# Kernel optimization log

Measured on AMD Instinct MI355X. Metric: run time of the kernel, lower is better.

## Reference

```python
import jax, jax.numpy as jnp
import numpy as np

GS_ITERS = 10
GS_TAU = 0.5
NEG = -1e9
B, L, D, H = 4, 512, 64, 128


def gphi_scores(x, W1, b1, W2, b2):
    # Faithful to: concat([x_i, x_j]) -> Linear(2D,H) -> ReLU -> Linear(H,1).squeeze(-1)
    # Linear on the concat of [x_i, x_j] == x_i @ W1[:D] + x_j @ W1[D:] (fused, no [B,L,L,2D] tensor).
    d = x.shape[-1]
    pi = jnp.einsum('bld,dh->blh', x, W1[:d])   # row-index half of concat
    pj = jnp.einsum('bld,dh->blh', x, W1[d:])   # col-index half of concat
    h = jax.nn.relu(pi[:, :, None, :] + pj[:, None, :, :] + b1)  # [B,L,L,H]
    return jnp.einsum('blmh,h->blm', h, W2[:, 0]) + b2[0]        # [B,L,L]


def gumbel_sinkhorn(log_alpha, gumbel, pad_mask, tau, n_iters):
    # (scores + gumbel noise)/tau, mask padded rows/cols, alternate row/col log-normalization.
    la = (log_alpha + gumbel) / tau
    la = jnp.where(pad_mask, NEG, la)

    def step(la, _):
        la = la - jax.nn.logsumexp(la, axis=2, keepdims=True)  # row normalize
        la = la - jax.nn.logsumexp(la, axis=1, keepdims=True)  # col normalize
        la = jnp.where(pad_mask, NEG, la)
        return la, None

    la, _ = jax.lax.scan(step, la, None, length=n_iters)
    return jnp.exp(la)


def make_pad_mask(seq_lens, max_len):
    # mask_map logic: for a sequence of length s, rows < s have cols < s valid; rows >= s fully invalid.
    ar = jnp.arange(max_len)
    s = seq_lens[:, None, None]
    valid = (ar[None, :, None] < s) & (ar[None, None, :] < s)
    return ~valid  # True where gumbel-masked


def setup_inputs() -> dict:
    key = jax.random.key(0)
    ks = jax.random.split(key, 8)
    event_time = jax.random.uniform(ks[0], (B, L), dtype=jnp.float32) * 10.0
    event_type = jax.random.randint(ks[1], (B, L), 0, 50, dtype=jnp.int32)
    clean_enc_out = jax.random.normal(ks[2], (B, L, D), dtype=jnp.float32)
    seq_lens = jax.random.randint(ks[3], (B,), 1, L + 1, dtype=jnp.int32)
    u = jax.random.uniform(ks[4], (B, L, L), dtype=jnp.float32, minval=1e-6, maxval=1.0 - 1e-6)
    gumbel_noise = -jnp.log(-jnp.log(u))
    # gphi_mlp params (xavier-ish scaling)
    W1 = jax.random.normal(ks[5], (2 * D, H), dtype=jnp.float32) * (1.0 / np.sqrt(2 * D))
    b1 = jnp.full((H,), 0.01, dtype=jnp.float32)
    W2 = jax.random.normal(ks[6], (H, 1), dtype=jnp.float32) * (1.0 / np.sqrt(H))
    b2 = jnp.full((1,), 0.01, dtype=jnp.float32)
    return {"event_time": event_time, "event_type": event_type,
            "clean_enc_out": clean_enc_out, "seq_lens": seq_lens,
            "gumbel_noise": gumbel_noise, "W1": W1, "b1": b1, "W2": W2, "b2": b2}


def reference(event_time, event_type, clean_enc_out, seq_lens, gumbel_noise, W1, b1, W2, b2):
    pad_mask = make_pad_mask(seq_lens, event_time.shape[1])
    scores = gphi_scores(clean_enc_out, W1, b1, W2, b2)           # [B,L,L]
    perm = gumbel_sinkhorn(scores, gumbel_noise, pad_mask, GS_TAU, GS_ITERS)
    # same_perm_matrix=True, no_time_noise=True path
    types_permed = jnp.einsum('bl,blm->bm', event_type.astype(jnp.float32), perm)
    times_permed = jnp.einsum('bl,blm->bm', event_time, perm)
    return types_permed, times_permed, perm
```

## Files before the change

### kernel.cpp

```cpp
#include <hip/hip_runtime.h>
#include <hip/hip_bf16.h>
#include <cstdint>

#define BB 4
#define LL 512
#define DD 64
#define HH 128
#define NEGV -1000000000.0f

__device__ __forceinline__ void fma4(float4& a, float s, const float4& w) {
    a.x += s * w.x; a.y += s * w.y; a.z += s * w.z; a.w += s * w.w;
}
__device__ __forceinline__ float4 f4max(const float4 a, const float4 b) {
    return make_float4(fmaxf(a.x,b.x), fmaxf(a.y,b.y), fmaxf(a.z,b.z), fmaxf(a.w,b.w));
}
__device__ __forceinline__ float4 f4add(const float4 a, const float4 b) {
    return make_float4(a.x+b.x, a.y+b.y, a.z+b.z, a.w+b.w);
}
__device__ __forceinline__ float4 f4expsub(const float4 v, const float4 m) {
    return make_float4(__expf(v.x-m.x), __expf(v.y-m.y), __expf(v.z-m.z), __expf(v.w-m.w));
}
__device__ __forceinline__ float4 f4mul(const float4 a, const float4 b) {
    return make_float4(a.x*b.x, a.y*b.y, a.z*b.z, a.w*b.w);
}
__device__ __forceinline__ float4 f4log(const float4 a) {
    return make_float4(__logf(a.x), __logf(a.y), __logf(a.z), __logf(a.w));
}

__global__ __launch_bounds__(256) void k_pipj(
    const float* __restrict__ x, const float* __restrict__ W1,
    const float* __restrict__ b1, float* __restrict__ pi, float* __restrict__ pj)
{
    int t = threadIdx.x;
    int hq = t & 63;
    int rr = t >> 6;
    int half = hq >> 5;
    int hc = (hq & 31) << 2;
    int row0 = blockIdx.x * 8 + rr;

    const float* Wb = W1 + half * 64 * HH + hc;
    float4 acc0;
    if (half == 0) acc0 = *(const float4*)(b1 + hc);
    else           acc0 = make_float4(0.f, 0.f, 0.f, 0.f);
    float4 acc1 = acc0;

    const float* x0 = x + (size_t)row0 * DD;
    const float* x1 = x + (size_t)(row0 + 4) * DD;
    #pragma unroll 4
    for (int dq = 0; dq < 16; ++dq) {
        float4 xa = *(const float4*)(x0 + (dq << 2));
        float4 xb = *(const float4*)(x1 + (dq << 2));
        float4 w0 = *(const float4*)(Wb + (dq*4 + 0) * HH);
        float4 w1 = *(const float4*)(Wb + (dq*4 + 1) * HH);
        float4 w2 = *(const float4*)(Wb + (dq*4 + 2) * HH);
        float4 w3 = *(const float4*)(Wb + (dq*4 + 3) * HH);
        fma4(acc0, xa.x, w0); fma4(acc0, xa.y, w1); fma4(acc0, xa.z, w2); fma4(acc0, xa.w, w3);
        fma4(acc1, xb.x, w0); fma4(acc1, xb.y, w1); fma4(acc1, xb.z, w2); fma4(acc1, xb.w, w3);
    }
    float* dst = half ? pj : pi;
    *(float4*)(dst + (size_t)row0 * HH + hc)       = acc0;
    *(float4*)(dst + (size_t)(row0 + 4) * HH + hc) = acc1;
}

__global__ __launch_bounds__(256) void k_scores(
    const float* __restrict__ pig, const float* __restrict__ pjg,
    const float* __restrict__ W2g, const float* __restrict__ b2g,
    const float* __restrict__ gum, const int* __restrict__ slens,
    float* __restrict__ la)
{
    __shared__ float sp[64 * HH];
    __shared__ float sq[64 * HH];
    __shared__ float sw2[HH];

    int t = threadIdx.x;
    int b = blockIdx.z;
    int i0 = blockIdx.y * 64;
    int j0 = blockIdx.x * 64;
    int rowb = b * LL + i0;
    int colb = b * LL + j0;

    #pragma unroll
    for (int k = 0; k < 8; ++k) {
        int flat = (k << 8) + t;
        int i = flat >> 5;
        int q = flat & 31;
        int dq = q ^ ((i >> 2) & 7);
        float4 va = *(const float4*)(pig + ((size_t)(rowb + i)) * HH + (q << 2));
        float4 vb = *(const float4*)(pjg + ((size_t)(colb + i)) * HH + (q << 2));
        *(float4*)(sp + i * HH + (dq << 2)) = va;
        *(float4*)(sq + i * HH + (dq << 2)) = vb;
    }
    if (t < HH) sw2[t] = W2g[t];
    __syncthreads();

    int w = t >> 6, lane = t & 63;
    int ti = ((w >> 1) << 3) + (lane >> 3);
    int tj = ((w & 1) << 3) + (lane & 7);
    int kti = ti & 7, ktj = tj & 7;

    float acc[4][4];
    #pragma unroll
    for (int a = 0; a < 4; ++a)
        #pragma unroll
        for (int c = 0; c < 4; ++c) acc[a][c] = 0.f;

    for (int hq = 0; hq < 32; ++hq) {
        float4 w4 = *(const float4*)(sw2 + (hq << 2));
        int offi = (hq ^ kti) << 2;
        int offj = (hq ^ ktj) << 2;
        float4 pa[4], pb[4];
        #pragma unroll
        for (int a = 0; a < 4; ++a) pa[a] = *(const float4*)(sp + (4*ti + a) * HH + offi);
        #pragma unroll
        for (int c = 0; c < 4; ++c) pb[c] = *(const float4*)(sq + (4*tj + c) * HH + offj);
        #pragma unroll
        for (int a = 0; a < 4; ++a) {
            #pragma unroll
            for (int c = 0; c < 4; ++c) {
                float t0 = fmaxf(pa[a].x + pb[c].x, 0.f);
                float t1 = fmaxf(pa[a].y + pb[c].y, 0.f);
                float t2 = fmaxf(pa[a].z + pb[c].z, 0.f);
                float t3 = fmaxf(pa[a].w + pb[c].w, 0.f);
                float s = acc[a][c];
                s += t0 * w4.x; s += t1 * w4.y; s += t2 * w4.z; s += t3 * w4.w;
                acc[a][c] = s;
            }
        }
    }

    int sl = slens[b];
    float bb2 = b2g[0];
    int jb = j0 + 4 * tj;
    #pragma unroll
    for (int a = 0; a < 4; ++a) {
        int ig = i0 + 4 * ti + a;
        float4 g = *(const float4*)(gum + ((size_t)(b * LL + ig)) * LL + jb);
        bool iv = ig < sl;
        float4 o;
        o.x = (iv && (jb + 0) < sl) ? (acc[a][0] + bb2 + g.x) * 2.0f : NEGV;
        o.y = (iv && (jb + 1) < sl) ? (acc[a][1] + bb2 + g.y) * 2.0f : NEGV;
        o.z = (iv && (jb + 2) < sl) ? (acc[a][2] + bb2 + g.z) * 2.0f : NEGV;
        o.w = (iv && (jb + 3) < sl) ? (acc[a][3] + bb2 + g.w) * 2.0f : NEGV;
        *(float4*)(la + ((size_t)(b * LL + ig)) * LL + jb) = o;
    }
}

__global__ __launch_bounds__(256) void k_rownorm(float* __restrict__ la)
{
    int wid = (blockIdx.x << 2) + (threadIdx.x >> 6);
    int lane = threadIdx.x & 63;
    float4* row = (float4*)(la + (size_t)wid * LL);
    float4 a = row[lane];
    float4 b = row[lane + 64];
    float m = fmaxf(fmaxf(fmaxf(a.x, a.y), fmaxf(a.z, a.w)),
                    fmaxf(fmaxf(b.x, b.y), fmaxf(b.z, b.w)));
    #pragma unroll
    for (int off = 32; off; off >>= 1) m = fmaxf(m, __shfl_xor(m, off));
    float s = __expf(a.x - m) + __expf(a.y - m) + __expf(a.z - m) + __expf(a.w - m)
            + __expf(b.x - m) + __expf(b.y - m) + __expf(b.z - m) + __expf(b.w - m);
    #pragma unroll
    for (int off = 32; off; off >>= 1) s += __shfl_xor(s, off);
    float lse = m + __logf(s);
    a.x -= lse; a.y -= lse; a.z -= lse; a.w -= lse;
    b.x -= lse; b.y -= lse; b.z -= lse; b.w -= lse;
    row[lane] = a;
    row[lane + 64] = b;
}

__global__ __launch_bounds__(1024) void k_colnorm(
    float* __restrict__ la, const int* __restrict__ slens,
    const int* __restrict__ etype, const float* __restrict__ etime,
    float* __restrict__ otype, float* __restrict__ otime, int last)
{
    __shared__ float4 Lm[1024];
    __shared__ float4 Ls[1024];
    __shared__ float4 clse[8];

    int t = threadIdx.x;
    int cg = t & 7;
    int rg = t >> 3;
    int b  = blockIdx.x >> 4;
    int j0 = (blockIdx.x & 15) << 5;

    float4* base = (float4*)(la + ((size_t)b * LL) * LL + j0);

    float4 v[4];
    #pragma unroll
    for (int k = 0; k < 4; ++k) v[k] = base[(size_t)(4 * rg + k) * 128 + cg];

    float4 m = f4max(f4max(v[0], v[1]), f4max(v[2], v[3]));
    float4 s = f4add(f4add(f4expsub(v[0], m), f4expsub(v[1], m)),
                     f4add(f4expsub(v[2], m), f4expsub(v[3], m)));
    Lm[t] = m; Ls[t] = s;
    __syncthreads();
    for (int off = 64; off >= 1; off >>= 1) {
        if (rg < off) {
            float4 m2 = Lm[((rg + off) << 3) + cg];
            float4 s2 = Ls[((rg + off) << 3) + cg];
            float4 nm = f4max(m, m2);
            s = f4add(f4mul(s, f4expsub(m, nm)), f4mul(s2, f4expsub(m2, nm)));
            m = nm;
            Lm[t] = m; Ls[t] = s;
        }
        __syncthreads();
    }
    if (rg == 0) clse[cg] = f4add(m, f4log(s));
    __syncthreads();
    float4 lse = clse[cg];

    int sl = slens[b];
    int jb = j0 + (cg << 2);
    bool jv0 = (jb + 0) < sl, jv1 = (jb + 1) < sl, jv2 = (jb + 2) < sl, jv3 = (jb + 3) < sl;

    if (!last) {
        #pragma unroll
        for (int k = 0; k < 4; ++k) {
            int i = 4 * rg + k;
            bool iv = i < sl;
            float4 o;
            o.x = (iv && jv0) ? v[k].x - lse.x : NEGV;
            o.y = (iv && jv1) ? v[k].y - lse.y : NEGV;
            o.z = (iv && jv2) ? v[k].z - lse.z : NEGV;
            o.w = (iv && jv3) ? v[k].w - lse.w : NEGV;
            base[(size_t)i * 128 + cg] = o;
        }
    } else {
        float4 ty = make_float4(0.f, 0.f, 0.f, 0.f);
        float4 tm = make_float4(0.f, 0.f, 0.f, 0.f);
        #pragma unroll
        for (int k = 0; k < 4; ++k) {
            int i = 4 * rg + k;
            bool iv = i < sl;
            float etf = (float)etype[b * LL + i];
            float etm = etime[b * LL + i];
            float4 p;
            p.x = (iv && jv0) ? __expf(v[k].x - lse.x) : 0.f;
            p.y = (iv && jv1) ? __expf(v[k].y - lse.y) : 0.f;
            p.z = (iv && jv2) ? __expf(v[k].z - lse.z) : 0.f;
            p.w = (iv && jv3) ? __expf(v[k].w - lse.w) : 0.f;
            base[(size_t)i * 128 + cg] = p;
            fma4(ty, etf, p);
            fma4(tm, etm, p);
        }
        Lm[t] = ty; Ls[t] = tm;
        __syncthreads();
        for (int off = 64; off >= 1; off >>= 1) {
            if (rg < off) {
                ty = f4add(ty, Lm[((rg + off) << 3) + cg]);
                tm = f4add(tm, Ls[((rg + off) << 3) + cg]);
                Lm[t] = ty; Ls[t] = tm;
            }
            __syncthreads();
        }
        if (rg == 0) {
            *(float4*)(otype + b * LL + jb) = ty;
            *(float4*)(otime + b * LL + jb) = tm;
        }
    }
}

extern "C" void kernel_launch(void* const* d_in, const int* in_sizes, int n_in,
                              void* d_out, int out_size, void* d_ws, size_t ws_size,
                              hipStream_t stream)
{
    const float* etime = (const float*)d_in[0];
    const int*   etype = (const int*)d_in[1];
    const float* x     = (const float*)d_in[2];
    const int*   slens = (const int*)d_in[3];
    const float* gum   = (const float*)d_in[4];
    const float* W1    = (const float*)d_in[5];
    const float* b1    = (const float*)d_in[6];
    const float* W2    = (const float*)d_in[7];
    const float* b2    = (const float*)d_in[8];

    float* out   = (float*)d_out;
    float* otype = out;
    float* otime = out + BB * LL;
    float* la    = out + 2 * BB * LL;
    float* pi = (float*)d_ws;
    float* pj = pi + (size_t)BB * LL * HH;

    k_pipj<<<256, 256, 0, stream>>>(x, W1, b1, pi, pj);
    k_scores<<<dim3(8, 8, BB), 256, 0, stream>>>(pi, pj, W2, b2, gum, slens, la);
    for (int it = 0; it < 10; ++it) {
        k_rownorm<<<512, 256, 0, stream>>>(la);
        k_colnorm<<<64, 1024, 0, stream>>>(la, slens, etype, etime, otype, otime,
                                           (it == 9) ? 1 : 0);
    }
}
```

Before: 133.9 us.

## Fuse whole pipeline into one cooperative persistent kernel with grid barriers

Replaces the 22 separate launches (projection, scores, and ten row/column normalisation pairs) with a single cooperative kernel using atomic grid barriers between phases. During Sinkhorn, 64 blocks each keep a 32-row stripe of the score matrix resident in shared memory. Row normalisation is done locally, and column log-sum-exp is combined through partial max/sum buffers in global memory with one grid barrier per iteration. This removes launch overhead and repeated global round trips of the 4MB matrix, at the cost of idle blocks during Sinkhorn, spin-barrier latency, and reliance on co-residency of 256 blocks of 1024 threads.

```diff
diff --git a/kernel.cpp b/kernel.cpp
--- a/kernel.cpp
+++ b/kernel.cpp
@@ -1,5 +1,4 @@
 #include <hip/hip_runtime.h>
-#include <hip/hip_bf16.h>
 #include <cstdint>
 
 #define BB 4
@@ -7,255 +6,318 @@
 #define DD 64
 #define HH 128
 #define NEGV -1000000000.0f
-
-__device__ __forceinline__ void fma4(float4& a, float s, const float4& w) {
-    a.x += s * w.x; a.y += s * w.y; a.z += s * w.z; a.w += s * w.w;
+#define NBLK 256
+#define NTHR 1024
+#define NACT 64
+
+__device__ __forceinline__ void grid_barrier(unsigned* cnt, unsigned target) {
+    __syncthreads();
+    if (threadIdx.x == 0) {
+        __hip_atomic_fetch_add(cnt, 1u, __ATOMIC_RELEASE, __HIP_MEMORY_SCOPE_AGENT);
+        while (__hip_atomic_load(cnt, __ATOMIC_ACQUIRE, __HIP_MEMORY_SCOPE_AGENT) < target)
+            __builtin_amdgcn_s_sleep(2);
+    }
+    __syncthreads();
 }
-__device__ __forceinline__ float4 f4max(const float4 a, const float4 b) {
-    return make_float4(fmaxf(a.x,b.x), fmaxf(a.y,b.y), fmaxf(a.z,b.z), fmaxf(a.w,b.w));
+
+__device__ __forceinline__ float hmax4(float4 v) {
+    return fmaxf(fmaxf(v.x, v.y), fmaxf(v.z, v.w));
 }
-__device__ __forceinline__ float4 f4add(const float4 a, const float4 b) {
-    return make_float4(a.x+b.x, a.y+b.y, a.z+b.z, a.w+b.w);
-}
-__device__ __forceinline__ float4 f4expsub(const float4 v, const float4 m) {
-    return make_float4(__expf(v.x-m.x), __expf(v.y-m.y), __expf(v.z-m.z), __expf(v.w-m.w));
-}
-__device__ __forceinline__ float4 f4mul(const float4 a, const float4 b) {
-    return make_float4(a.x*b.x, a.y*b.y, a.z*b.z, a.w*b.w);
-}
-__device__ __forceinline__ float4 f4log(const float4 a) {
-    return make_float4(__logf(a.x), __logf(a.y), __logf(a.z), __logf(a.w));
-}
-
-__global__ __launch_bounds__(256) void k_pipj(
-    const float* __restrict__ x, const float* __restrict__ W1,
-    const float* __restrict__ b1, float* __restrict__ pi, float* __restrict__ pj)
+
+__global__ __launch_bounds__(NTHR) void mega(
+    const float* __restrict__ etime, const int* __restrict__ etype,
+    const float* __restrict__ x, const int* __restrict__ slens,
+    const float* __restrict__ gum, const float* __restrict__ W1,
+    const float* __restrict__ b1, const float* __restrict__ W2,
+    const float* __restrict__ b2, float* __restrict__ out, float* __restrict__ ws)
 {
-    int t = threadIdx.x;
-    int hq = t & 63;
-    int rr = t >> 6;
-    int half = hq >> 5;
-    int hc = (hq & 31) << 2;
-    int row0 = blockIdx.x * 8 + rr;
-
-    const float* Wb = W1 + half * 64 * HH + hc;
-    float4 acc0;
-    if (half == 0) acc0 = *(const float4*)(b1 + hc);
-    else           acc0 = make_float4(0.f, 0.f, 0.f, 0.f);
-    float4 acc1 = acc0;
-
-    const float* x0 = x + (size_t)row0 * DD;
-    const float* x1 = x + (size_t)(row0 + 4) * DD;
-    #pragma unroll 4
-    for (int dq = 0; dq < 16; ++dq) {
-        float4 xa = *(const float4*)(x0 + (dq << 2));
-        float4 xb = *(const float4*)(x1 + (dq << 2));
-        float4 w0 = *(const float4*)(Wb + (dq*4 + 0) * HH);
-        float4 w1 = *(const float4*)(Wb + (dq*4 + 1) * HH);
-        float4 w2 = *(const float4*)(Wb + (dq*4 + 2) * HH);
-        float4 w3 = *(const float4*)(Wb + (dq*4 + 3) * HH);
-        fma4(acc0, xa.x, w0); fma4(acc0, xa.y, w1); fma4(acc0, xa.z, w2); fma4(acc0, xa.w, w3);
-        fma4(acc1, xb.x, w0); fma4(acc1, xb.y, w1); fma4(acc1, xb.z, w2); fma4(acc1, xb.w, w3);
-    }
-    float* dst = half ? pj : pi;
-    *(float4*)(dst + (size_t)row0 * HH + hc)       = acc0;
-    *(float4*)(dst + (size_t)(row0 + 4) * HH + hc) = acc1;
-}
-
-__global__ __launch_bounds__(256) void k_scores(
-    const float* __restrict__ pig, const float* __restrict__ pjg,
-    const float* __restrict__ W2g, const float* __restrict__ b2g,
-    const float* __restrict__ gum, const int* __restrict__ slens,
-    float* __restrict__ la)
-{
-    __shared__ float sp[64 * HH];
-    __shared__ float sq[64 * HH];
-    __shared__ float sw2[HH];
-
-    int t = threadIdx.x;
-    int b = blockIdx.z;
-    int i0 = blockIdx.y * 64;
-    int j0 = blockIdx.x * 64;
-    int rowb = b * LL + i0;
-    int colb = b * LL + j0;
-
-    #pragma unroll
-    for (int k = 0; k < 8; ++k) {
-        int flat = (k << 8) + t;
-        int i = flat >> 5;
-        int q = flat & 31;
-        int dq = q ^ ((i >> 2) & 7);
-        float4 va = *(const float4*)(pig + ((size_t)(rowb + i)) * HH + (q << 2));
-        float4 vb = *(const float4*)(pjg + ((size_t)(colb + i)) * HH + (q << 2));
-        *(float4*)(sp + i * HH + (dq << 2)) = va;
-        *(float4*)(sq + i * HH + (dq << 2)) = vb;
-    }
-    if (t < HH) sw2[t] = W2g[t];
-    __syncthreads();
-
-    int w = t >> 6, lane = t & 63;
-    int ti = ((w >> 1) << 3) + (lane >> 3);
-    int tj = ((w & 1) << 3) + (lane & 7);
-    int kti = ti & 7, ktj = tj & 7;
-
-    float acc[4][4];
-    #pragma unroll
-    for (int a = 0; a < 4; ++a)
-        #pragma unroll
-        for (int c = 0; c < 4; ++c) acc[a][c] = 0.f;
-
-    for (int hq = 0; hq < 32; ++hq) {
-        float4 w4 = *(const float4*)(sw2 + (hq << 2));
-        int offi = (hq ^ kti) << 2;
-        int offj = (hq ^ ktj) << 2;
-        float4 pa[4], pb[4];
-        #pragma unroll
-        for (int a = 0; a < 4; ++a) pa[a] = *(const float4*)(sp + (4*ti + a) * HH + offi);
-        #pragma unroll
-        for (int c = 0; c < 4; ++c) pb[c] = *(const float4*)(sq + (4*tj + c) * HH + offj);
-        #pragma unroll
-        for (int a = 0; a < 4; ++a) {
-            #pragma unroll
-            for (int c = 0; c < 4; ++c) {
-                float t0 = fmaxf(pa[a].x + pb[c].x, 0.f);
-                float t1 = fmaxf(pa[a].y + pb[c].y, 0.f);
-                float t2 = fmaxf(pa[a].z + pb[c].z, 0.f);
-                float t3 = fmaxf(pa[a].w + pb[c].w, 0.f);
-                float s = acc[a][c];
-                s += t0 * w4.x; s += t1 * w4.y; s += t2 * w4.z; s += t3 * w4.w;
-                acc[a][c] = s;
+    __shared__ float smem[19072];
+
+    unsigned* cnt = (unsigned*)ws;
+    float* piG  = ws + 64;
+    float* pjG  = piG + BB * LL * HH;
+    float* laG  = pjG + BB * LL * HH;
+    float* cmG  = laG + (size_t)BB * LL * LL;
+    float* csG  = cmG + 2 * BB * 32 * LL;
+    float* otyG = csG + 2 * BB * 32 * LL;
+    float* otmG = otyG + BB * 16 * LL;
+
+    const int t = threadIdx.x;
+    const int bx = blockIdx.x;
+
+    {
+        int gid = (bx << 10) + t;
+        int row = gid >> 7;
+        int h = gid & (HH - 1);
+        const float* xr = x + row * DD;
+        float ap = b1[h];
+        float aq = 0.f;
+        #pragma unroll 8
+        for (int d = 0; d < DD; ++d) {
+            float xv = xr[d];
+            ap = fmaf(xv, W1[d * HH + h], ap);
+            aq = fmaf(xv, W1[(DD + d) * HH + h], aq);
+        }
+        piG[row * HH + h] = ap;
+        pjG[row * HH + h] = aq;
+    }
+    grid_barrier(cnt, 1 * NBLK);
+
+    {
+        float* sp  = smem;
+        float* sq  = smem + 8192;
+        float* sw2 = smem + 18944;
+        int jt = bx & 7, it8 = (bx >> 3) & 7, b = bx >> 6;
+        int i0 = it8 << 6, j0 = jt << 6;
+        int rowb = b * LL + i0, colb = b * LL + j0;
+
+        #pragma unroll
+        for (int k = 0; k < 2; ++k) {
+            int flat = (k << 10) + t;
+            int i = flat >> 5, q = flat & 31;
+            int dq = q ^ ((i >> 2) & 7);
+            *(float4*)(sp + i * HH + (dq << 2)) =
+                *(const float4*)(piG + (size_t)(rowb + i) * HH + (q << 2));
+            *(float4*)(sq + i * HH + (dq << 2)) =
+                *(const float4*)(pjG + (size_t)(colb + i) * HH + (q << 2));
+        }
+        if (t < HH) sw2[t] = W2[t];
+        __syncthreads();
+
+        int hg = t >> 8, tt = t & 255;
+        int w = tt >> 6, lane = tt & 63;
+        int ti = ((w >> 1) << 3) + (lane >> 3);
+        int tj = ((w & 1) << 3) + (lane & 7);
+        int kti = ti & 7, ktj = tj & 7;
+
+        float acc[4][4];
+        #pragma unroll
+        for (int a = 0; a < 4; ++a)
+            #pragma unroll
+            for (int c = 0; c < 4; ++c) acc[a][c] = 0.f;
+
+        for (int hq = hg * 8; hq < hg * 8 + 8; ++hq) {
+            float4 w4 = *(const float4*)(sw2 + (hq << 2));
+            int offi = (hq ^ kti) << 2;
+            int offj = (hq ^ ktj) << 2;
+            float4 pa[4], pb[4];
+            #pragma unroll
+            for (int a = 0; a < 4; ++a) pa[a] = *(const float4*)(sp + (4*ti + a) * HH + offi);
+            #pragma unroll
+            for (int c = 0; c < 4; ++c) pb[c] = *(const float4*)(sq + (4*tj + c) * HH + offj);
+            #pragma unroll
+            for (int a = 0; a < 4; ++a) {
+                #pragma unroll
+                for (int c = 0; c < 4; ++c) {
+                    float t0 = fmaxf(pa[a].x + pb[c].x, 0.f);
+                    float t1 = fmaxf(pa[a].y + pb[c].y, 0.f);
+                    float t2 = fmaxf(pa[a].z + pb[c].z, 0.f);
+                    float t3 = fmaxf(pa[a].w + pb[c].w, 0.f);
+                    float s = acc[a][c];
+                    s += t0 * w4.x; s += t1 * w4.y; s += t2 * w4.z; s += t3 * w4.w;
+                    acc[a][c] = s;
+                }
             }
         }
-    }
-
-    int sl = slens[b];
-    float bb2 = b2g[0];
-    int jb = j0 + 4 * tj;
-    #pragma unroll
-    for (int a = 0; a < 4; ++a) {
-        int ig = i0 + 4 * ti + a;
-        float4 g = *(const float4*)(gum + ((size_t)(b * LL + ig)) * LL + jb);
+        __syncthreads();
+        float* cbuf = smem;
+        #pragma unroll
+        for (int a = 0; a < 4; ++a)
+            #pragma unroll
+            for (int c = 0; c < 4; ++c)
+                cbuf[(((hg << 8) + tt) << 4) + (a << 2) + c] = acc[a][c];
+        __syncthreads();
+
+        int tt2 = t >> 2, a2 = t & 3;
+        int w2_ = tt2 >> 6, lane2 = tt2 & 63;
+        int ti2 = ((w2_ >> 1) << 3) + (lane2 >> 3);
+        int tj2 = ((w2_ & 1) << 3) + (lane2 & 7);
+        float4 o = make_float4(0.f, 0.f, 0.f, 0.f);
+        #pragma unroll
+        for (int g = 0; g < 4; ++g) {
+            float4 pp = *(const float4*)(cbuf + (((g << 8) + tt2) << 4) + (a2 << 2));
+            o.x += pp.x; o.y += pp.y; o.z += pp.z; o.w += pp.w;
+        }
+        int sl = slens[b];
+        float bb2 = b2[0];
+        int ig = i0 + 4 * ti2 + a2;
+        int jb = j0 + 4 * tj2;
+        float4 g4 = *(const float4*)(gum + ((size_t)(b * LL + ig)) * LL + jb);
         bool iv = ig < sl;
-        float4 o;
-        o.x = (iv && (jb + 0) < sl) ? (acc[a][0] + bb2 + g.x) * 2.0f : NEGV;
-        o.y = (iv && (jb + 1) < sl) ? (acc[a][1] + bb2 + g.y) * 2.0f : NEGV;
-        o.z = (iv && (jb + 2) < sl) ? (acc[a][2] + bb2 + g.z) * 2.0f : NEGV;
-        o.w = (iv && (jb + 3) < sl) ? (acc[a][3] + bb2 + g.w) * 2.0f : NEGV;
-        *(float4*)(la + ((size_t)(b * LL + ig)) * LL + jb) = o;
-    }
-}
-
-__global__ __launch_bounds__(256) void k_rownorm(float* __restrict__ la)
-{
-    int wid = (blockIdx.x << 2) + (threadIdx.x >> 6);
-    int lane = threadIdx.x & 63;
-    float4* row = (float4*)(la + (size_t)wid * LL);
-    float4 a = row[lane];
-    float4 b = row[lane + 64];
-    float m = fmaxf(fmaxf(fmaxf(a.x, a.y), fmaxf(a.z, a.w)),
-                    fmaxf(fmaxf(b.x, b.y), fmaxf(b.z, b.w)));
-    #pragma unroll
-    for (int off = 32; off; off >>= 1) m = fmaxf(m, __shfl_xor(m, off));
-    float s = __expf(a.x - m) + __expf(a.y - m) + __expf(a.z - m) + __expf(a.w - m)
-            + __expf(b.x - m) + __expf(b.y - m) + __expf(b.z - m) + __expf(b.w - m);
-    #pragma unroll
-    for (int off = 32; off; off >>= 1) s += __shfl_xor(s, off);
-    float lse = m + __logf(s);
-    a.x -= lse; a.y -= lse; a.z -= lse; a.w -= lse;
-    b.x -= lse; b.y -= lse; b.z -= lse; b.w -= lse;
-    row[lane] = a;
-    row[lane + 64] = b;
-}
-
-__global__ __launch_bounds__(1024) void k_colnorm(
-    float* __restrict__ la, const int* __restrict__ slens,
-    const int* __restrict__ etype, const float* __restrict__ etime,
-    float* __restrict__ otype, float* __restrict__ otime, int last)
-{
-    __shared__ float4 Lm[1024];
-    __shared__ float4 Ls[1024];
-    __shared__ float4 clse[8];
-
-    int t = threadIdx.x;
-    int cg = t & 7;
-    int rg = t >> 3;
-    int b  = blockIdx.x >> 4;
-    int j0 = (blockIdx.x & 15) << 5;
-
-    float4* base = (float4*)(la + ((size_t)b * LL) * LL + j0);
-
-    float4 v[4];
-    #pragma unroll
-    for (int k = 0; k < 4; ++k) v[k] = base[(size_t)(4 * rg + k) * 128 + cg];
-
-    float4 m = f4max(f4max(v[0], v[1]), f4max(v[2], v[3]));
-    float4 s = f4add(f4add(f4expsub(v[0], m), f4expsub(v[1], m)),
-                     f4add(f4expsub(v[2], m), f4expsub(v[3], m)));
-    Lm[t] = m; Ls[t] = s;
-    __syncthreads();
-    for (int off = 64; off >= 1; off >>= 1) {
-        if (rg < off) {
-            float4 m2 = Lm[((rg + off) << 3) + cg];
-            float4 s2 = Ls[((rg + off) << 3) + cg];
-            float4 nm = f4max(m, m2);
-            s = f4add(f4mul(s, f4expsub(m, nm)), f4mul(s2, f4expsub(m2, nm)));
-            m = nm;
-            Lm[t] = m; Ls[t] = s;
-        }
+        float4 res;
+        res.x = (iv && (jb + 0) < sl) ? (o.x + bb2 + g4.x) * 2.0f : NEGV;
+        res.y = (iv && (jb + 1) < sl) ? (o.y + bb2 + g4.y) * 2.0f : NEGV;
+        res.z = (iv && (jb + 2) < sl) ? (o.z + bb2 + g4.z) * 2.0f : NEGV;
+        res.w = (iv && (jb + 3) < sl) ? (o.w + bb2 + g4.w) * 2.0f : NEGV;
+        *(float4*)(laG + ((size_t)(b * LL + ig)) * LL + jb) = res;
+    }
+    grid_barrier(cnt, 2 * NBLK);
+
+    const bool active = bx < NACT;
+    const int b2i = bx >> 4;
+    const int stripe = bx & 15;
+    const int r0 = stripe << 5;
+    float* sla  = smem;
+    float* redm = smem + 16384;
+    float* reds = smem + 17408;
+    float* clse = smem + 18432;
+    int sl_a = 0;
+
+    if (active) {
+        sl_a = slens[b2i];
+        float4* sla4 = (float4*)sla;
+        const float4* src4 = (const float4*)(laG + (((size_t)(b2i << 9) + r0) << 9));
+        #pragma unroll
+        for (int k = 0; k < 4; ++k) sla4[(k << 10) + t] = src4[(k << 10) + t];
         __syncthreads();
     }
-    if (rg == 0) clse[cg] = f4add(m, f4log(s));
-    __syncthreads();
-    float4 lse = clse[cg];
-
-    int sl = slens[b];
-    int jb = j0 + (cg << 2);
-    bool jv0 = (jb + 0) < sl, jv1 = (jb + 1) < sl, jv2 = (jb + 2) < sl, jv3 = (jb + 3) < sl;
-
-    if (!last) {
-        #pragma unroll
-        for (int k = 0; k < 4; ++k) {
-            int i = 4 * rg + k;
-            bool iv = i < sl;
-            float4 o;
-            o.x = (iv && jv0) ? v[k].x - lse.x : NEGV;
-            o.y = (iv && jv1) ? v[k].y - lse.y : NEGV;
-            o.z = (iv && jv2) ? v[k].z - lse.z : NEGV;
-            o.w = (iv && jv3) ? v[k].w - lse.w : NEGV;
-            base[(size_t)i * 128 + cg] = o;
-        }
-    } else {
-        float4 ty = make_float4(0.f, 0.f, 0.f, 0.f);
-        float4 tm = make_float4(0.f, 0.f, 0.f, 0.f);
-        #pragma unroll
-        for (int k = 0; k < 4; ++k) {
-            int i = 4 * rg + k;
-            bool iv = i < sl;
-            float etf = (float)etype[b * LL + i];
-            float etm = etime[b * LL + i];
-            float4 p;
-            p.x = (iv && jv0) ? __expf(v[k].x - lse.x) : 0.f;
-            p.y = (iv && jv1) ? __expf(v[k].y - lse.y) : 0.f;
-            p.z = (iv && jv2) ? __expf(v[k].z - lse.z) : 0.f;
-            p.w = (iv && jv3) ? __expf(v[k].w - lse.w) : 0.f;
-            base[(size_t)i * 128 + cg] = p;
-            fma4(ty, etf, p);
-            fma4(tm, etm, p);
-        }
-        Lm[t] = ty; Ls[t] = tm;
-        __syncthreads();
-        for (int off = 64; off >= 1; off >>= 1) {
-            if (rg < off) {
-                ty = f4add(ty, Lm[((rg + off) << 3) + cg]);
-                tm = f4add(tm, Ls[((rg + off) << 3) + cg]);
-                Lm[t] = ty; Ls[t] = tm;
+
+    for (int it = 0; it < 10; ++it) {
+        const int par = it & 1;
+        const int last = (it == 9);
+        if (active) {
+            int r = t >> 5, cq = t & 31;
+            float4 v[4];
+            #pragma unroll
+            for (int k = 0; k < 4; ++k)
+                v[k] = *(float4*)(sla + (r << 9) + ((cq + (k << 5)) << 2));
+            float m = fmaxf(fmaxf(hmax4(v[0]), hmax4(v[1])), fmaxf(hmax4(v[2]), hmax4(v[3])));
+            #pragma unroll
+            for (int off = 16; off; off >>= 1) m = fmaxf(m, __shfl_xor(m, off));
+            float s = 0.f;
+            #pragma unroll
+            for (int k = 0; k < 4; ++k)
+                s += __expf(v[k].x - m) + __expf(v[k].y - m) + __expf(v[k].z - m) + __expf(v[k].w - m);
+            #pragma unroll
+            for (int off = 16; off; off >>= 1) s += __shfl_xor(s, off);
+            float lse = m + __logf(s);
+            #pragma unroll
+            for (int k = 0; k < 4; ++k) {
+                v[k].x -= lse; v[k].y -= lse; v[k].z -= lse; v[k].w -= lse;
+                *(float4*)(sla + (r << 9) + ((cq + (k << 5)) << 2)) = v[k];
             }
             __syncthreads();
-        }
-        if (rg == 0) {
-            *(float4*)(otype + b * LL + jb) = ty;
-            *(float4*)(otime + b * LL + jb) = tm;
-        }
+
+            int c = t & 511, half = t >> 9;
+            float vv[16];
+            #pragma unroll
+            for (int rr = 0; rr < 16; ++rr) vv[rr] = sla[(((half << 4) + rr) << 9) + c];
+            float mp = vv[0];
+            #pragma unroll
+            for (int rr = 1; rr < 16; ++rr) mp = fmaxf(mp, vv[rr]);
+            float spv = 0.f;
+            #pragma unroll
+            for (int rr = 0; rr < 16; ++rr) spv += __expf(vv[rr] - mp);
+            size_t pidx = ((((size_t)par * BB + b2i) << 5) + (stripe << 1) + half) * LL + c;
+            cmG[pidx] = mp;
+            csG[pidx] = spv;
+        }
+        grid_barrier(cnt, (3 + it) * NBLK);
+        if (active) {
+            int c = t & 511, half = t >> 9;
+            const float* cmB = cmG + ((((size_t)par * BB + b2i) << 5)) * LL;
+            const float* csB = csG + ((((size_t)par * BB + b2i) << 5)) * LL;
+            int g0 = half << 4;
+            float mreg[16];
+            #pragma unroll
+            for (int g = 0; g < 16; ++g) mreg[g] = cmB[(g0 + g) * LL + c];
+            float M = mreg[0];
+            #pragma unroll
+            for (int g = 1; g < 16; ++g) M = fmaxf(M, mreg[g]);
+            redm[(half << 9) + c] = M;
+            __syncthreads();
+            float Mg = fmaxf(redm[c], redm[512 + c]);
+            float S = 0.f;
+            #pragma unroll
+            for (int g = 0; g < 16; ++g)
+                S = fmaf(csB[(g0 + g) * LL + c], __expf(mreg[g] - Mg), S);
+            reds[(half << 9) + c] = S;
+            __syncthreads();
+            if (half == 0) clse[c] = Mg + __logf(reds[c] + reds[512 + c]);
+            __syncthreads();
+
+            int r = t >> 5, cq = t & 31;
+            int grow = r0 + r;
+            bool ivR = grow < sl_a;
+            if (!last) {
+                #pragma unroll
+                for (int k = 0; k < 4; ++k) {
+                    int cb = (cq + (k << 5)) << 2;
+                    float4 v = *(float4*)(sla + (r << 9) + cb);
+                    float4 l = *(const float4*)(clse + cb);
+                    float4 o;
+                    o.x = (ivR && (cb + 0) < sl_a) ? v.x - l.x : NEGV;
+                    o.y = (ivR && (cb + 1) < sl_a) ? v.y - l.y : NEGV;
+                    o.z = (ivR && (cb + 2) < sl_a) ? v.z - l.z : NEGV;
+                    o.w = (ivR && (cb + 3) < sl_a) ? v.w - l.w : NEGV;
+                    *(float4*)(sla + (r << 9) + cb) = o;
+                }
+            } else {
+                float etf = (float)etype[(b2i << 9) + grow];
+                float etv = etime[(b2i << 9) + grow];
+                float4 p[4];
+                #pragma unroll
+                for (int k = 0; k < 4; ++k) {
+                    int cb = (cq + (k << 5)) << 2;
+                    float4 v = *(float4*)(sla + (r << 9) + cb);
+                    float4 l = *(const float4*)(clse + cb);
+                    float4 q;
+                    q.x = (ivR && (cb + 0) < sl_a) ? __expf(v.x - l.x) : 0.f;
+                    q.y = (ivR && (cb + 1) < sl_a) ? __expf(v.y - l.y) : 0.f;
+                    q.z = (ivR && (cb + 2) < sl_a) ? __expf(v.z - l.z) : 0.f;
+                    q.w = (ivR && (cb + 3) < sl_a) ? __expf(v.w - l.w) : 0.f;
+                    p[k] = q;
+                    *(float4*)(out + 2 * BB * LL + (((size_t)(b2i << 9) + grow) << 9) + cb) = q;
+                }
+                #pragma unroll
+                for (int k = 0; k < 4; ++k) {
+                    int cb = (cq + (k << 5)) << 2;
+                    *(float4*)(sla + (r << 9) + cb) =
+                        make_float4(p[k].x * etf, p[k].y * etf, p[k].z * etf, p[k].w * etf);
+                }
+                __syncthreads();
+                {
+                    int c2 = t & 511, h2 = t >> 9;
+                    float sA = 0.f;
+                    #pragma unroll
+                    for (int rr = 0; rr < 16; ++rr) sA += sla[(((h2 << 4) + rr) << 9) + c2];
+                    redm[(h2 << 9) + c2] = sA;
+                }
+                __syncthreads();
+                if (t < 512) otyG[((b2i << 4) + stripe) * LL + t] = redm[t] + redm[512 + t];
+                __syncthreads();
+                #pragma unroll
+                for (int k = 0; k < 4; ++k) {
+                    int cb = (cq + (k << 5)) << 2;
+                    *(float4*)(sla + (r << 9) + cb) =
+                        make_float4(p[k].x * etv, p[k].y * etv, p[k].z * etv, p[k].w * etv);
+                }
+                __syncthreads();
+                {
+                    int c2 = t & 511, h2 = t >> 9;
+                    float sB = 0.f;
+                    #pragma unroll
+                    for (int rr = 0; rr < 16; ++rr) sB += sla[(((h2 << 4) + rr) << 9) + c2];
+                    reds[(h2 << 9) + c2] = sB;
+                }
+                __syncthreads();
+                if (t < 512) otmG[((b2i << 4) + stripe) * LL + t] = reds[t] + reds[512 + t];
+            }
+        }
+    }
+    grid_barrier(cnt, 13 * NBLK);
+
+    if (bx < 64 && t < 32) {
+        int b = bx >> 4, chunk = bx & 15;
+        int c = (chunk << 5) + t;
+        float a = 0.f, d = 0.f;
+        #pragma unroll
+        for (int s = 0; s < 16; ++s) {
+            a += otyG[((b << 4) + s) * LL + c];
+            d += otmG[((b << 4) + s) * LL + c];
+        }
+        out[(b << 9) + c] = a;
+        out[BB * LL + (b << 9) + c] = d;
     }
 }
 
@@ -272,19 +334,16 @@
     const float* b1    = (const float*)d_in[6];
     const float* W2    = (const float*)d_in[7];
     const float* b2    = (const float*)d_in[8];
-
-    float* out   = (float*)d_out;
-    float* otype = out;
-    float* otime = out + BB * LL;
-    float* la    = out + 2 * BB * LL;
-    float* pi = (float*)d_ws;
-    float* pj = pi + (size_t)BB * LL * HH;
-
-    k_pipj<<<256, 256, 0, stream>>>(x, W1, b1, pi, pj);
-    k_scores<<<dim3(8, 8, BB), 256, 0, stream>>>(pi, pj, W2, b2, gum, slens, la);
-    for (int it = 0; it < 10; ++it) {
-        k_rownorm<<<512, 256, 0, stream>>>(la);
-        k_colnorm<<<64, 1024, 0, stream>>>(la, slens, etype, etime, otype, otime,
-                                           (it == 9) ? 1 : 0);
+    float* out = (float*)d_out;
+    float* wsf = (float*)d_ws;
+
+    hipMemsetAsync(d_ws, 0, 256, stream);
+
+    void* args[] = {(void*)&etime, (void*)&etype, (void*)&x, (void*)&slens, (void*)&gum,
+                    (void*)&W1, (void*)&b1, (void*)&W2, (void*)&b2, (void*)&out, (void*)&wsf};
+    hipError_t err = hipLaunchCooperativeKernel((const void*)mega, dim3(NBLK), dim3(NTHR),
+                                                args, 0, stream);
+    if (err != hipSuccess) {
+        mega<<<NBLK, NTHR, 0, stream>>>(etime, etype, x, slens, gum, W1, b1, W2, b2, out, wsf);
     }
 }
```

Result: slower. 336.6 us (+151.3%).
